# Performance work log

Measured on AMD Instinct MI355X. Metric: run time of the kernel, lower is better.

## Reference

```python
import jax, jax.numpy as jnp
import numpy as np

N = 500_000          # number of particles
D = 6                # phase-space dimension
N_BINS = 128         # bins per axis
SQRT2 = 1.4142135623730951
BANDWIDTH = 1.0      # kernel width relative to bin width (module default)


def setup_inputs() -> dict:
    key = jax.random.key(0)
    x = jax.random.normal(key, (N, D), dtype=jnp.float32)
    edges = jnp.linspace(-3.0, 3.0, N_BINS + 1, dtype=jnp.float32)
    return {"x": x, "bin_edges_x": edges, "bin_edges_y": edges}


def _cdf_weights(u, edges, bw):
    """Per-point Gaussian mass in each bin via CDF (erf) differences.

    u: (n,), edges: (m+1,) -> weights (n, m); row sums <= 1.
    """
    z = jax.scipy.special.erf((edges[None, :] - u[:, None]) / (bw * SQRT2))  # (n, m+1)
    return 0.5 * (z[:, 1:] - z[:, :-1])  # (n, m)


def reference(x, bin_edges_x, bin_edges_y):
    dx = bin_edges_x[1] - bin_edges_x[0]
    dy = bin_edges_y[1] - bin_edges_y[0]
    bw_x = BANDWIDTH * dx
    bw_y = BANDWIDTH * dy
    # axis = (0, 1): project onto first two phase-space coordinates
    wx = _cdf_weights(x[:, 0], bin_edges_x, bw_x)  # (n, bx)
    wy = _cdf_weights(x[:, 1], bin_edges_y, bw_y)  # (n, by)
    hist = jnp.einsum('ni,nj->ij', wx, wy)         # (bx, by)
    # normalize to a probability density over the grid
    hist = hist / (hist.sum() * dx * dy)
    return hist
```

## Files before the change

### kernel.cpp

```cpp
#include <hip/hip_runtime.h>
#include <math.h>


#define NBINS   128
#define NB2     (NBINS * NBINS)
#define KC      256
#define AX_B    32768
#define THREADS 512
#define NBLOCKS 512
#define QSCALE  320.0f

typedef int i32x4 __attribute__((ext_vector_type(4)));

static __device__ __forceinline__ unsigned short f2bf(float f) {
    unsigned int b = __float_as_uint(f);
    b += 0x7fff + ((b >> 16) & 1);
    return (unsigned short)(b >> 16);
}
static __device__ __forceinline__ float bf2f(unsigned short u) {
    return __uint_as_float((unsigned int)u << 16);
}

static __device__ __forceinline__ float erf_fast(float x) {
    const float ax = fabsf(x);
    const float t  = __builtin_amdgcn_rcpf(fmaf(0.3275911f, ax, 1.0f));
    const float e  = __expf(-x * x);
    float p = fmaf(1.061405429f, t, -1.453152027f);
    p = fmaf(p, t, 1.421413741f);
    p = fmaf(p, t, -0.284496736f);
    p = fmaf(p, t, 0.254829592f);
    p = p * t;
    return copysignf(fmaf(-p, e, 1.0f), x);
}

__global__ __launch_bounds__(THREADS, 4) void hist_mfma_kernel(
    const float* __restrict__ x,
    const float* __restrict__ edges_x,
    const float* __restrict__ edges_y,
    unsigned short* __restrict__ partials,
    float* __restrict__ btot,
    int n)
{
    __shared__ __align__(16) signed char sh[2 * AX_B];
    __shared__ int xw[8];

    const int tid  = threadIdx.x;
    const int lane = tid & 63;
    const int wv   = tid >> 6;

    const float e0x = edges_x[0];
    const float dxw = edges_x[1] - e0x;
    const float e0y = edges_y[0];
    const float dyw = edges_y[1] - e0y;

    const int axis = tid >> 8;
    const int pl   = tid & 255;
    const float e0   = axis ? e0y : e0x;
    const float invd = 1.0f / (axis ? dyw : dxw);
    const float cc   = 0.7071067811865476f;
    signed char* const sdst =
        sh + axis * AX_B + (pl >> 6) * 1024 + ((pl >> 4) & 3) * 256 + (pl & 15);

    i32x4 acc[4][4];
    #pragma unroll
    for (int i = 0; i < 4; ++i)
        #pragma unroll
        for (int j = 0; j < 4; ++j)
            acc[i][j] = (i32x4){0, 0, 0, 0};

    const int rowQ = ((wv >> 1) & 1) * 4;
    const int colQ = (wv & 1) * 4;
    const int ks0  = (wv >> 2) * 2;

    const int nchunks = (n + KC - 1) / KC;

    float u = 1e30f;
    {
        const int p = blockIdx.x * KC + pl;
        if (blockIdx.x < nchunks && p < n) u = x[(size_t)p * 6 + axis];
    }
    int b0;
    signed char qv[8];
    {
        const float spos = (u - e0) * invd;
        int b = (int)floorf(spos + 0.5f) - 4;
        b0 = b < 0 ? 0 : (b > NBINS - 8 ? NBINS - 8 : b);
        const float t0 = ((float)b0 - spos) * cc;
        float z[9];
        #pragma unroll
        for (int k = 0; k < 9; ++k) z[k] = erf_fast(t0 + (float)k * cc);
        #pragma unroll
        for (int k = 0; k < 8; ++k)
            qv[k] = (signed char)(int)rintf(0.5f * (z[k + 1] - z[k]) * QSCALE);
    }
    int oldb0 = b0;

    {
        float4* zp = (float4*)sh;
        #pragma unroll
        for (int i = 0; i < 8; ++i)
            zp[tid + i * THREADS] = (float4){0.f, 0.f, 0.f, 0.f};
    }
    __syncthreads();

    for (int chunk = blockIdx.x; chunk < nchunks; chunk += gridDim.x) {
        const int nchunk = chunk + gridDim.x;
        float un = 1e30f;
        if (nchunk < nchunks) {
            const int pn = nchunk * KC + pl;
            if (pn < n) un = x[(size_t)pn * 6 + axis];
        }

        #pragma unroll
        for (int k = 0; k < 8; ++k) {
            const int b = oldb0 + k;
            sdst[(b >> 4) * 4096 + (b & 15) * 16] = 0;
        }
        #pragma unroll
        for (int k = 0; k < 8; ++k) {
            const int b = b0 + k;
            sdst[(b >> 4) * 4096 + (b & 15) * 16] = qv[k];
        }
        __syncthreads();

        #pragma unroll
        for (int s = 0; s < 2; ++s) {
            const int ks = ks0 + s;
            i32x4 av[4], bv[4];
            #pragma unroll
            for (int i = 0; i < 4; ++i)
                av[i] = *(const i32x4*)(sh + (rowQ + i) * 4096 + ks * 1024 + lane * 16);
            #pragma unroll
            for (int j = 0; j < 4; ++j)
                bv[j] = *(const i32x4*)(sh + AX_B + (colQ + j) * 4096 + ks * 1024 + lane * 16);
            #pragma unroll
            for (int i = 0; i < 4; ++i)
                #pragma unroll
                for (int j = 0; j < 4; ++j)
                    acc[i][j] = __builtin_amdgcn_mfma_i32_16x16x64_i8(
                        av[i], bv[j], acc[i][j], 0, 0, 0);
        }

        {
            oldb0 = b0;
            const float spos = (un - e0) * invd;
            int b = (int)floorf(spos + 0.5f) - 4;
            b0 = b < 0 ? 0 : (b > NBINS - 8 ? NBINS - 8 : b);
            const float t0 = ((float)b0 - spos) * cc;
            float z[9];
            #pragma unroll
            for (int k = 0; k < 9; ++k) z[k] = erf_fast(t0 + (float)k * cc);
            #pragma unroll
            for (int k = 0; k < 8; ++k)
                qv[k] = (signed char)(int)rintf(0.5f * (z[k + 1] - z[k]) * QSCALE);
        }
        __syncthreads();
    }

    if (wv >= 4) {
        int* dst = (int*)sh + (wv - 4) * 4096;
        #pragma unroll
        for (int i = 0; i < 4; ++i)
            #pragma unroll
            for (int j = 0; j < 4; ++j)
                #pragma unroll
                for (int g = 0; g < 4; ++g)
                    dst[((i * 4 + j) * 4 + g) * 64 + lane] = acc[i][j][g];
    }
    __syncthreads();

    int bsum = 0;
    if (wv < 4) {
        const float qs = 1.0f / (QSCALE * QSCALE);
        const int* src = (const int*)sh + wv * 4096;
        unsigned short* my = partials + (size_t)blockIdx.x * NB2;
        const int r0 = (lane >> 4) * 4;
        const int c0 = lane & 15;
        #pragma unroll
        for (int i = 0; i < 4; ++i)
            #pragma unroll
            for (int j = 0; j < 4; ++j)
                #pragma unroll
                for (int g = 0; g < 4; ++g) {
                    const int v = acc[i][j][g] + src[((i * 4 + j) * 4 + g) * 64 + lane];
                    bsum += v;
                    const int row = (rowQ + i) * 16 + r0 + g;
                    const int col = (colQ + j) * 16 + c0;
                    my[row * NBINS + col] = f2bf((float)v * qs);
                }
    }
    #pragma unroll
    for (int off = 32; off > 0; off >>= 1) bsum += __shfl_down(bsum, off, 64);
    if (lane == 0) xw[wv] = bsum;
    __syncthreads();
    if (tid == 0) {
        const float qs = 1.0f / (QSCALE * QSCALE);
        btot[blockIdx.x] = (float)(xw[0] + xw[1] + xw[2] + xw[3]) * qs;
    }
}

__global__ void reduce_kernel(const unsigned short* __restrict__ partials,
                              const float* __restrict__ btot,
                              const float* __restrict__ edges_x,
                              const float* __restrict__ edges_y,
                              float* __restrict__ out)
{
    __shared__ float4 red[16][16];
    __shared__ float ws[4];
    __shared__ float stot;

    const int t = threadIdx.x;
    const int bin4 = t & 15;
    const int pg = t >> 4;
    const int binBase = blockIdx.x * 64;

    float tl = btot[t] + btot[t + 256];
    #pragma unroll
    for (int off = 32; off > 0; off >>= 1) tl += __shfl_down(tl, off, 64);
    if ((t & 63) == 0) ws[t >> 6] = tl;

    const unsigned short* p =
        partials + (size_t)(pg * 32) * NB2 + binBase + bin4 * 4;
    float4 s = {0.f, 0.f, 0.f, 0.f};
    #pragma unroll 8
    for (int k = 0; k < 32; ++k) {
        const ushort4 v = *(const ushort4*)(p + (size_t)k * NB2);
        s.x += bf2f(v.x); s.y += bf2f(v.y); s.z += bf2f(v.z); s.w += bf2f(v.w);
    }
    red[pg][bin4] = s;
    __syncthreads();

    if (t == 0) {
        const float dxw = edges_x[1] - edges_x[0];
        const float dyw = edges_y[1] - edges_y[0];
        stot = 1.0f / ((ws[0] + ws[1] + ws[2] + ws[3]) * dxw * dyw);
    }
    __syncthreads();

    if (t < 16) {
        float4 a = red[0][t];
        #pragma unroll
        for (int g = 1; g < 16; ++g) {
            const float4 b = red[g][t];
            a.x += b.x; a.y += b.y; a.z += b.z; a.w += b.w;
        }
        a.x *= stot; a.y *= stot; a.z *= stot; a.w *= stot;
        *(float4*)(out + binBase + t * 4) = a;
    }
}

extern "C" void kernel_launch(void* const* d_in, const int* in_sizes, int n_in,
                              void* d_out, int out_size, void* d_ws, size_t ws_size,
                              hipStream_t stream)
{
    const float* x  = (const float*)d_in[0];
    const float* ex = (const float*)d_in[1];
    const float* ey = (const float*)d_in[2];
    float* out = (float*)d_out;
    const int n = in_sizes[0] / 6;

    unsigned short* partials = (unsigned short*)d_ws;
    float* btot = (float*)((char*)d_ws + (size_t)NBLOCKS * NB2 * 2);

    hist_mfma_kernel<<<NBLOCKS, THREADS, 0, stream>>>(x, ex, ey, partials, btot, n);
    reduce_kernel<<<NB2 / 64, 256, 0, stream>>>(partials, btot, ex, ey, out);
}
```

Measured before the change: 84.55 us.

## Replace per-block bf16 partials with int atomic accumulation into shared slots

Instead of each block writing a full bf16 partial histogram and a separate kernel reducing 512 of them, blocks atomically add integer counts into 32 slot histograms, which a small norm kernel sums and scales. This cuts the partial-histogram write and read traffic, and the integer sums also remove the bf16 rounding. In exchange it adds a zeroing kernel launch and millions of global atomics that may contend.

```diff
diff --git a/kernel.cpp b/kernel.cpp
--- a/kernel.cpp
+++ b/kernel.cpp
@@ -8,18 +8,10 @@
 #define AX_B    32768
 #define THREADS 512
 #define NBLOCKS 512
+#define NSLOTS  32
 #define QSCALE  320.0f
 
 typedef int i32x4 __attribute__((ext_vector_type(4)));
-
-static __device__ __forceinline__ unsigned short f2bf(float f) {
-    unsigned int b = __float_as_uint(f);
-    b += 0x7fff + ((b >> 16) & 1);
-    return (unsigned short)(b >> 16);
-}
-static __device__ __forceinline__ float bf2f(unsigned short u) {
-    return __uint_as_float((unsigned int)u << 16);
-}
 
 static __device__ __forceinline__ float erf_fast(float x) {
     const float ax = fabsf(x);
@@ -37,7 +29,7 @@
     const float* __restrict__ x,
     const float* __restrict__ edges_x,
     const float* __restrict__ edges_y,
-    unsigned short* __restrict__ partials,
+    int* __restrict__ slots,
     float* __restrict__ btot,
     int n)
 {
@@ -171,9 +163,8 @@
 
     int bsum = 0;
     if (wv < 4) {
-        const float qs = 1.0f / (QSCALE * QSCALE);
         const int* src = (const int*)sh + wv * 4096;
-        unsigned short* my = partials + (size_t)blockIdx.x * NB2;
+        int* slot = slots + (blockIdx.x & (NSLOTS - 1)) * NB2;
         const int r0 = (lane >> 4) * 4;
         const int c0 = lane & 15;
         #pragma unroll
@@ -186,7 +177,7 @@
                     bsum += v;
                     const int row = (rowQ + i) * 16 + r0 + g;
                     const int col = (colQ + j) * 16 + c0;
-                    my[row * NBINS + col] = f2bf((float)v * qs);
+                    atomicAdd(&slot[row * NBINS + col], v);
                 }
     }
     #pragma unroll
@@ -199,54 +190,47 @@
     }
 }
 
-__global__ void reduce_kernel(const unsigned short* __restrict__ partials,
-                              const float* __restrict__ btot,
-                              const float* __restrict__ edges_x,
-                              const float* __restrict__ edges_y,
-                              float* __restrict__ out)
-{
-    __shared__ float4 red[16][16];
-    __shared__ float ws[4];
+__global__ void zero_kernel(int4* __restrict__ slots)
+{
+    const int t = blockIdx.x * 256 + threadIdx.x;
+    slots[t] = (int4){0, 0, 0, 0};
+    slots[t + 256 * 256] = (int4){0, 0, 0, 0};
+}
+
+__global__ void norm_kernel(const int* __restrict__ slots,
+                            const float* __restrict__ btot,
+                            const float* __restrict__ edges_x,
+                            const float* __restrict__ edges_y,
+                            float* __restrict__ out)
+{
+    __shared__ float ws[8];
     __shared__ float stot;
 
     const int t = threadIdx.x;
-    const int bin4 = t & 15;
-    const int pg = t >> 4;
-    const int binBase = blockIdx.x * 64;
-
-    float tl = btot[t] + btot[t + 256];
+    const int bin = blockIdx.x * 512 + t;
+
+    float tl = btot[t];
     #pragma unroll
     for (int off = 32; off > 0; off >>= 1) tl += __shfl_down(tl, off, 64);
     if ((t & 63) == 0) ws[t >> 6] = tl;
 
-    const unsigned short* p =
-        partials + (size_t)(pg * 32) * NB2 + binBase + bin4 * 4;
-    float4 s = {0.f, 0.f, 0.f, 0.f};
-    #pragma unroll 8
-    for (int k = 0; k < 32; ++k) {
-        const ushort4 v = *(const ushort4*)(p + (size_t)k * NB2);
-        s.x += bf2f(v.x); s.y += bf2f(v.y); s.z += bf2f(v.z); s.w += bf2f(v.w);
-    }
-    red[pg][bin4] = s;
+    int v = 0;
+    #pragma unroll
+    for (int s = 0; s < NSLOTS; ++s) v += slots[s * NB2 + bin];
     __syncthreads();
 
     if (t == 0) {
         const float dxw = edges_x[1] - edges_x[0];
         const float dyw = edges_y[1] - edges_y[0];
-        stot = 1.0f / ((ws[0] + ws[1] + ws[2] + ws[3]) * dxw * dyw);
-    }
-    __syncthreads();
-
-    if (t < 16) {
-        float4 a = red[0][t];
-        #pragma unroll
-        for (int g = 1; g < 16; ++g) {
-            const float4 b = red[g][t];
-            a.x += b.x; a.y += b.y; a.z += b.z; a.w += b.w;
-        }
-        a.x *= stot; a.y *= stot; a.z *= stot; a.w *= stot;
-        *(float4*)(out + binBase + t * 4) = a;
-    }
+        float tot = 0.f;
+        #pragma unroll
+        for (int k = 0; k < 8; ++k) tot += ws[k];
+        stot = 1.0f / (tot * dxw * dyw);
+    }
+    __syncthreads();
+
+    const float qs = 1.0f / (QSCALE * QSCALE);
+    out[bin] = (float)v * qs * stot;
 }
 
 extern "C" void kernel_launch(void* const* d_in, const int* in_sizes, int n_in,
@@ -259,9 +243,10 @@
     float* out = (float*)d_out;
     const int n = in_sizes[0] / 6;
 
-    unsigned short* partials = (unsigned short*)d_ws;
-    float* btot = (float*)((char*)d_ws + (size_t)NBLOCKS * NB2 * 2);
-
-    hist_mfma_kernel<<<NBLOCKS, THREADS, 0, stream>>>(x, ex, ey, partials, btot, n);
-    reduce_kernel<<<NB2 / 64, 256, 0, stream>>>(partials, btot, ex, ey, out);
-}
+    int* slots = (int*)d_ws;
+    float* btot = (float*)((char*)d_ws + (size_t)NSLOTS * NB2 * 4);
+
+    zero_kernel<<<256, 256, 0, stream>>>((int4*)slots);
+    hist_mfma_kernel<<<NBLOCKS, THREADS, 0, stream>>>(x, ex, ey, slots, btot, n);
+    norm_kernel<<<NB2 / 512, 512, 0, stream>>>(slots, btot, ex, ey, out);
+}
```

Measured after the change: 97.20 us. 15.0% more time.

## Halve chunk size, double threads, give each wave a 2x2 output tile

Applied to the files above, without the earlier changes.

The chunk size drops to 128 particles per iteration and the block grows to 1024 threads. Each of the 16 waves now owns a 2x2 tile of 16x16 MFMA outputs over the full K range, so there is no K split. This removes the cross-wave reduction of accumulators through LDS at the end and halves LDS per block. The cost is twice as many loop iterations and barriers per point, with only 4 of 16 waves doing the erf and scatter work each chunk. Fewer accumulator registers per wave allow higher occupancy.

```diff
diff --git a/kernel.cpp b/kernel.cpp
--- a/kernel.cpp
+++ b/kernel.cpp
@@ -4,9 +4,9 @@
 
 #define NBINS   128
 #define NB2     (NBINS * NBINS)
-#define KC      256
-#define AX_B    32768
-#define THREADS 512
+#define KC      128
+#define AX_B    16384
+#define THREADS 1024
 #define NBLOCKS 512
 #define QSCALE  320.0f
 
@@ -33,7 +33,7 @@
     return copysignf(fmaf(-p, e, 1.0f), x);
 }
 
-__global__ __launch_bounds__(THREADS, 4) void hist_mfma_kernel(
+__global__ __launch_bounds__(THREADS, 8) void hist_mfma_kernel(
     const float* __restrict__ x,
     const float* __restrict__ edges_x,
     const float* __restrict__ edges_y,
@@ -42,7 +42,7 @@
     int n)
 {
     __shared__ __align__(16) signed char sh[2 * AX_B];
-    __shared__ int xw[8];
+    __shared__ int xw[16];
 
     const int tid  = threadIdx.x;
     const int lane = tid & 63;
@@ -53,35 +53,33 @@
     const float e0y = edges_y[0];
     const float dyw = edges_y[1] - e0y;
 
-    const int axis = tid >> 8;
-    const int pl   = tid & 255;
+    const bool isrole = (wv < 4);
+    const int axis = (tid >> 7) & 1;
+    const int pl   = tid & 127;
     const float e0   = axis ? e0y : e0x;
     const float invd = 1.0f / (axis ? dyw : dxw);
     const float cc   = 0.7071067811865476f;
     signed char* const sdst =
         sh + axis * AX_B + (pl >> 6) * 1024 + ((pl >> 4) & 3) * 256 + (pl & 15);
 
-    i32x4 acc[4][4];
+    const int rowT = (wv & 3) * 2;
+    const int colT = (wv >> 2) * 2;
+
+    i32x4 acc[2][2];
     #pragma unroll
-    for (int i = 0; i < 4; ++i)
-        #pragma unroll
-        for (int j = 0; j < 4; ++j)
+    for (int i = 0; i < 2; ++i)
+        #pragma unroll
+        for (int j = 0; j < 2; ++j)
             acc[i][j] = (i32x4){0, 0, 0, 0};
 
-    const int rowQ = ((wv >> 1) & 1) * 4;
-    const int colQ = (wv & 1) * 4;
-    const int ks0  = (wv >> 2) * 2;
-
     const int nchunks = (n + KC - 1) / KC;
 
-    float u = 1e30f;
-    {
+    int b0 = 0, oldb0 = 0;
+    signed char qv[8];
+    if (isrole) {
+        float u = 1e30f;
         const int p = blockIdx.x * KC + pl;
         if (blockIdx.x < nchunks && p < n) u = x[(size_t)p * 6 + axis];
-    }
-    int b0;
-    signed char qv[8];
-    {
         const float spos = (u - e0) * invd;
         int b = (int)floorf(spos + 0.5f) - 4;
         b0 = b < 0 ? 0 : (b > NBINS - 8 ? NBINS - 8 : b);
@@ -92,56 +90,55 @@
         #pragma unroll
         for (int k = 0; k < 8; ++k)
             qv[k] = (signed char)(int)rintf(0.5f * (z[k + 1] - z[k]) * QSCALE);
-    }
-    int oldb0 = b0;
+        oldb0 = b0;
+    }
 
     {
         float4* zp = (float4*)sh;
-        #pragma unroll
-        for (int i = 0; i < 8; ++i)
-            zp[tid + i * THREADS] = (float4){0.f, 0.f, 0.f, 0.f};
+        zp[tid] = (float4){0.f, 0.f, 0.f, 0.f};
+        zp[tid + THREADS] = (float4){0.f, 0.f, 0.f, 0.f};
     }
     __syncthreads();
 
     for (int chunk = blockIdx.x; chunk < nchunks; chunk += gridDim.x) {
+        if (isrole) {
+            #pragma unroll
+            for (int k = 0; k < 8; ++k) {
+                const int b = oldb0 + k;
+                sdst[(b >> 4) * 2048 + (b & 15) * 16] = 0;
+            }
+            #pragma unroll
+            for (int k = 0; k < 8; ++k) {
+                const int b = b0 + k;
+                sdst[(b >> 4) * 2048 + (b & 15) * 16] = qv[k];
+            }
+        }
+        __syncthreads();
+
+        float un = 1e30f;
         const int nchunk = chunk + gridDim.x;
-        float un = 1e30f;
-        if (nchunk < nchunks) {
+        if (isrole && nchunk < nchunks) {
             const int pn = nchunk * KC + pl;
             if (pn < n) un = x[(size_t)pn * 6 + axis];
         }
 
         #pragma unroll
-        for (int k = 0; k < 8; ++k) {
-            const int b = oldb0 + k;
-            sdst[(b >> 4) * 4096 + (b & 15) * 16] = 0;
-        }
-        #pragma unroll
-        for (int k = 0; k < 8; ++k) {
-            const int b = b0 + k;
-            sdst[(b >> 4) * 4096 + (b & 15) * 16] = qv[k];
-        }
-        __syncthreads();
-
-        #pragma unroll
         for (int s = 0; s < 2; ++s) {
-            const int ks = ks0 + s;
-            i32x4 av[4], bv[4];
-            #pragma unroll
-            for (int i = 0; i < 4; ++i)
-                av[i] = *(const i32x4*)(sh + (rowQ + i) * 4096 + ks * 1024 + lane * 16);
-            #pragma unroll
-            for (int j = 0; j < 4; ++j)
-                bv[j] = *(const i32x4*)(sh + AX_B + (colQ + j) * 4096 + ks * 1024 + lane * 16);
-            #pragma unroll
-            for (int i = 0; i < 4; ++i)
+            i32x4 av[2];
+            #pragma unroll
+            for (int i = 0; i < 2; ++i)
+                av[i] = *(const i32x4*)(sh + (rowT + i) * 2048 + s * 1024 + lane * 16);
+            #pragma unroll
+            for (int j = 0; j < 2; ++j) {
+                const i32x4 bv = *(const i32x4*)(sh + AX_B + (colT + j) * 2048 + s * 1024 + lane * 16);
                 #pragma unroll
-                for (int j = 0; j < 4; ++j)
+                for (int i = 0; i < 2; ++i)
                     acc[i][j] = __builtin_amdgcn_mfma_i32_16x16x64_i8(
-                        av[i], bv[j], acc[i][j], 0, 0, 0);
-        }
-
-        {
+                        av[i], bv, acc[i][j], 0, 0, 0);
+            }
+        }
+
+        if (isrole) {
             oldb0 = b0;
             const float spos = (un - e0) * invd;
             int b = (int)floorf(spos + 0.5f) - 4;
@@ -157,35 +154,22 @@
         __syncthreads();
     }
 
-    if (wv >= 4) {
-        int* dst = (int*)sh + (wv - 4) * 4096;
-        #pragma unroll
-        for (int i = 0; i < 4; ++i)
-            #pragma unroll
-            for (int j = 0; j < 4; ++j)
-                #pragma unroll
-                for (int g = 0; g < 4; ++g)
-                    dst[((i * 4 + j) * 4 + g) * 64 + lane] = acc[i][j][g];
-    }
-    __syncthreads();
-
     int bsum = 0;
-    if (wv < 4) {
+    {
         const float qs = 1.0f / (QSCALE * QSCALE);
-        const int* src = (const int*)sh + wv * 4096;
         unsigned short* my = partials + (size_t)blockIdx.x * NB2;
         const int r0 = (lane >> 4) * 4;
         const int c0 = lane & 15;
         #pragma unroll
-        for (int i = 0; i < 4; ++i)
-            #pragma unroll
-            for (int j = 0; j < 4; ++j)
+        for (int i = 0; i < 2; ++i)
+            #pragma unroll
+            for (int j = 0; j < 2; ++j)
                 #pragma unroll
                 for (int g = 0; g < 4; ++g) {
-                    const int v = acc[i][j][g] + src[((i * 4 + j) * 4 + g) * 64 + lane];
+                    const int v = acc[i][j][g];
                     bsum += v;
-                    const int row = (rowQ + i) * 16 + r0 + g;
-                    const int col = (colQ + j) * 16 + c0;
+                    const int row = (rowT + i) * 16 + r0 + g;
+                    const int col = (colT + j) * 16 + c0;
                     my[row * NBINS + col] = f2bf((float)v * qs);
                 }
     }
@@ -195,7 +179,10 @@
     __syncthreads();
     if (tid == 0) {
         const float qs = 1.0f / (QSCALE * QSCALE);
-        btot[blockIdx.x] = (float)(xw[0] + xw[1] + xw[2] + xw[3]) * qs;
+        int s = 0;
+        #pragma unroll
+        for (int k = 0; k < 16; ++k) s += xw[k];
+        btot[blockIdx.x] = (float)s * qs;
     }
 }
 
```

After: 85.12 us. No clear change (+0.7%).
